# Optimization experiments

Hardware: AMD Instinct MI355X
Metric: run time of the kernel (lower is better)

The kernel has to match this reference:

```python
import jax, jax.numpy as jnp
import numpy as np

N, E, F, DH, R = 50000, 800000, 128, 128, 6  # nodes, edges, in-feat, hidden, relations (heads=1)
EPS = 1e-5
NEG_SLOPE = 0.01


def setup_inputs() -> dict:
    key = jax.random.key(0)
    ks = jax.random.split(key, 20)
    sF = 1.0 / np.sqrt(F)
    sD = 1.0 / np.sqrt(DH)
    return {
        "x": jax.random.normal(ks[0], (N, F), dtype=jnp.float32),
        "edge_index": jax.random.randint(ks[1], (2, E), 0, N, dtype=jnp.int64),
        "edge_type": jax.random.randint(ks[2], (E,), 0, R, dtype=jnp.int64),
        # RGCNConv params
        "rgcn_w": jax.random.normal(ks[3], (R, F, DH), dtype=jnp.float32) * sF,
        "rgcn_root": jax.random.normal(ks[4], (F, DH), dtype=jnp.float32) * sF,
        "rgcn_bias": jnp.zeros((DH,), dtype=jnp.float32),
        # TransformerConv params (heads=1, concat=True)
        "wq": jax.random.normal(ks[5], (DH, DH), dtype=jnp.float32) * sD,
        "bq": jnp.zeros((DH,), dtype=jnp.float32),
        "wk": jax.random.normal(ks[6], (DH, DH), dtype=jnp.float32) * sD,
        "bk": jnp.zeros((DH,), dtype=jnp.float32),
        "wv": jax.random.normal(ks[7], (DH, DH), dtype=jnp.float32) * sD,
        "bv": jnp.zeros((DH,), dtype=jnp.float32),
        "wskip": jax.random.normal(ks[8], (DH, DH), dtype=jnp.float32) * sD,
        "bskip": jnp.zeros((DH,), dtype=jnp.float32),
        # BatchNorm1d params (training-mode batch stats)
        "bn_gamma": jnp.ones((DH,), dtype=jnp.float32),
        "bn_beta": jnp.zeros((DH,), dtype=jnp.float32),
    }


def _rgcn(x, src, dst, edge_type, w, root, bias):
    # PyG RGCNConv: per-relation mean aggregation of x_j @ W_r over incoming edges, + root + bias
    out = x @ root + bias  # [N, DH]
    for r in range(R):
        m = (edge_type == r)
        xw = x @ w[r]  # [N, DH]
        msg = jnp.where(m[:, None], xw[src], 0.0)  # [E, DH]
        s = jax.ops.segment_sum(msg, dst, num_segments=N)
        cnt = jax.ops.segment_sum(m.astype(x.dtype), dst, num_segments=N)
        out = out + s / jnp.maximum(cnt, 1.0)[:, None]
    return out


def _transformer_conv(x, src, dst, wq, bq, wk, bk, wv, bv, wskip, bskip):
    # PyG TransformerConv, heads=1: edge-softmax attention over incoming edges + skip projection
    q = x @ wq + bq  # [N, DH]
    k = x @ wk + bk
    v = x @ wv + bv
    score = jnp.sum(q[dst] * k[src], axis=-1) / jnp.sqrt(jnp.asarray(DH, x.dtype))  # [E]
    smax = jax.ops.segment_max(score, dst, num_segments=N)  # -inf for empty segments (unused)
    a = jnp.exp(score - smax[dst])
    denom = jax.ops.segment_sum(a, dst, num_segments=N)
    alpha = a / denom[dst]  # every edge's dst has >=1 edge, denom > 0
    agg = jax.ops.segment_sum(alpha[:, None] * v[src], dst, num_segments=N)  # [N, DH]
    return agg + (x @ wskip + bskip)


def reference(x, edge_index, edge_type, rgcn_w, rgcn_root, rgcn_bias,
              wq, bq, wk, bk, wv, bv, wskip, bskip, bn_gamma, bn_beta):
    src, dst = edge_index[0], edge_index[1]
    h = _rgcn(x, src, dst, edge_type, rgcn_w, rgcn_root, rgcn_bias)
    h = _transformer_conv(h, src, dst, wq, bq, wk, bk, wv, bv, wskip, bskip)
    # BatchNorm1d (training: batch statistics, biased variance)
    mu = jnp.mean(h, axis=0)
    var = jnp.mean(jnp.square(h - mu), axis=0)
    h = bn_gamma * (h - mu) * jax.lax.rsqrt(var + EPS) + bn_beta
    return jnp.where(h > 0, h, NEG_SLOPE * h)
```

## Files before the change

### kernel.cpp

```cpp
#include <hip/hip_runtime.h>
#include <hip/hip_bf16.h>
#include <math.h>

#define FDIM 128
#define NREL 6

typedef _Float16 half8 __attribute__((ext_vector_type(8)));
typedef _Float16 h16x2 __attribute__((ext_vector_type(2)));
typedef float f32x4 __attribute__((ext_vector_type(4)));

#if __has_builtin(__builtin_amdgcn_fdot2)
#define FDOT2(A, B, C) __builtin_amdgcn_fdot2((A), (B), (C), false)
#else
#define FDOT2(A, B, C) ((float)(A)[0] * (float)(B)[0] + ((float)(A)[1] * (float)(B)[1] + (C)))
#endif

static __device__ __forceinline__ unsigned short f2h(float f) {
  union { _Float16 h; unsigned short u; } p; p.h = (_Float16)f; return p.u;
}

__global__ void cvt_x_kernel(const float* __restrict__ x, unsigned short* __restrict__ xh,
                             int n4) {
  int i = blockIdx.x * 256 + threadIdx.x;
  if (i < n4) {
    float4 v = ((const float4*)x)[i];
    union { _Float16 h[4]; uint2 u; } p;
    p.h[0] = (_Float16)v.x; p.h[1] = (_Float16)v.y;
    p.h[2] = (_Float16)v.z; p.h[3] = (_Float16)v.w;
    ((uint2*)xh)[i] = p.u;
  }
}

__global__ void cvt_wr_kernel(const float* __restrict__ root, const float* __restrict__ w,
                              unsigned short* __restrict__ bt) {
  int i = blockIdx.x * 256 + threadIdx.x;
  if (i < 896 * 128) {
    int n = i / 896, kk = i - n * 896;
    float v = (kk < 128) ? root[kk * 128 + n] : w[(long long)(kk - 128) * 128 + n];
    bt[i] = f2h(v);
  }
}

struct WPtrs { const float* W[4]; };
__global__ void cvt_wq_kernel(WPtrs wp, unsigned short* __restrict__ bt) {
  int i = blockIdx.x * 256 + threadIdx.x;
  if (i < 4 * 128 * 128) {
    int z = i >> 14;
    int r = i & 16383;
    int n = r >> 7, kk = r & 127;
    bt[i] = f2h(wp.W[z][kk * 128 + n]);
  }
}

struct GArgs {
  const unsigned short* Ax;
  const unsigned short* Aagg;
  const unsigned short* Bt;
  const float* bias[4];
  unsigned short* qh; unsigned short* kh; unsigned short* vh; float* sk;
  unsigned short* h;
  int M, K;
};

template <int MODE>
__launch_bounds__(256)
__global__ void gemm_mfma(GArgs g) {
  __shared__ unsigned short Ah[64 * 64];
  __shared__ unsigned short Bh[128 * 64];
  const int tid = threadIdx.x;
  const int lane = tid & 63;
  const int wid = tid >> 6;
  const int wm = wid >> 1, wn = wid & 1;
  const int lr = lane & 15, lk = lane >> 4;
  const int m0 = blockIdx.x * 64;
  const int z = (MODE == 1) ? blockIdx.z : 0;
  const unsigned short* Bt = g.Bt + (long long)z * 128 * g.K;
  const int K = g.K;
  const int M = g.M;

  f32x4 acc[2][4];
#pragma unroll
  for (int a = 0; a < 2; ++a)
#pragma unroll
    for (int b = 0; b < 4; ++b) { acc[a][b][0] = 0.f; acc[a][b][1] = 0.f; acc[a][b][2] = 0.f; acc[a][b][3] = 0.f; }

  for (int k0 = 0; k0 < K; k0 += 64) {
    __syncthreads();
#pragma unroll
    for (int p = 0; p < 2; ++p) {
      int idx = tid + 256 * p;
      int r = idx >> 3, c = idx & 7;
      int row = m0 + r; if (row > M - 1) row = M - 1;
      const unsigned short* srcp;
      if (MODE == 0)
        srcp = (k0 < 128) ? (g.Ax + (long long)row * 128 + k0 + c * 8)
                          : (g.Aagg + (long long)row * 768 + (k0 - 128) + c * 8);
      else
        srcp = g.Ax + (long long)row * 128 + k0 + c * 8;
      uint4 u = *(const uint4*)srcp;
      ((uint4*)Ah)[r * 8 + (c ^ (r & 7))] = u;
    }
#pragma unroll
    for (int p = 0; p < 4; ++p) {
      int idx = tid + 256 * p;
      int rn = idx >> 3, c = idx & 7;
      uint4 u = *(const uint4*)(Bt + (long long)rn * K + k0 + c * 8);
      ((uint4*)Bh)[rn * 8 + (c ^ (rn & 7))] = u;
    }
    __syncthreads();
#pragma unroll
    for (int ks = 0; ks < 2; ++ks) {
      half8 a[2], b[4];
#pragma unroll
      for (int fm = 0; fm < 2; ++fm) {
        int row = wm * 32 + fm * 16 + lr;
        a[fm] = *(const half8*)&((uint4*)Ah)[row * 8 + ((ks * 4 + lk) ^ (row & 7))];
      }
#pragma unroll
      for (int fn = 0; fn < 4; ++fn) {
        int col = wn * 64 + fn * 16 + lr;
        b[fn] = *(const half8*)&((uint4*)Bh)[col * 8 + ((ks * 4 + lk) ^ (col & 7))];
      }
#pragma unroll
      for (int fm = 0; fm < 2; ++fm)
#pragma unroll
        for (int fn = 0; fn < 4; ++fn)
          acc[fm][fn] = __builtin_amdgcn_mfma_f32_16x16x32_f16(a[fm], b[fn], acc[fm][fn], 0, 0, 0);
    }
  }

  const float CF = 0.08838834764831845f * 1.4426950408889634f;
  const float* bias = (MODE == 0) ? g.bias[0] : g.bias[z];
#pragma unroll
  for (int fm = 0; fm < 2; ++fm) {
#pragma unroll
    for (int fn = 0; fn < 4; ++fn) {
      int col = wn * 64 + fn * 16 + lr;
      float bv = bias[col];
#pragma unroll
      for (int j = 0; j < 4; ++j) {
        int row = m0 + wm * 32 + fm * 16 + lk * 4 + j;
        if (row < M) {
          float vv = acc[fm][fn][j] + bv;
          long long off = (long long)row * 128 + col;
          if (MODE == 0) {
            g.h[off] = f2h(vv);
          } else {
            if (z == 0) g.qh[off] = f2h(vv * CF);
            else if (z == 1) g.kh[off] = f2h(vv);
            else if (z == 2) g.vh[off] = f2h(vv);
            else g.sk[off] = vv;
          }
        }
      }
    }
  }
}

__global__ void hist_kernel(const int* __restrict__ dst, const int* __restrict__ etype,
                            int* __restrict__ cnt, int E) {
  int e = blockIdx.x * blockDim.x + threadIdx.x;
  if (e < E) atomicAdd(&cnt[dst[e] * NREL + etype[e]], 1);
}

__launch_bounds__(1024)
__global__ void scan1(const int* __restrict__ deg, int* __restrict__ incl,
                      int* __restrict__ part, int n) {
  __shared__ int sh[1024];
  int tid = threadIdx.x;
  int i = blockIdx.x * 1024 + tid;
  sh[tid] = (i < n) ? deg[i] : 0;
  __syncthreads();
  for (int o = 1; o < 1024; o <<= 1) {
    int t = (tid >= o) ? sh[tid - o] : 0;
    __syncthreads();
    sh[tid] += t;
    __syncthreads();
  }
  if (i < n) incl[i] = sh[tid];
  if (tid == 1023) part[blockIdx.x] = sh[1023];
}

__global__ void scan2(int* part, int nb) {
  int lane = threadIdx.x;
  int run = 0;
  for (int b0 = 0; b0 < nb; b0 += 64) {
    int i = b0 + lane;
    int orig = (i < nb) ? part[i] : 0;
    int v = orig;
#pragma unroll
    for (int o = 1; o < 64; o <<= 1) {
      int t = __shfl_up(v, o);
      if (lane >= o) v += t;
    }
    if (i < nb) part[i] = run + v - orig;
    run += __shfl(v, 63);
  }
}

__global__ void scan3(const int* __restrict__ incl, const int* __restrict__ part,
                      int* __restrict__ offs, int n) {
  int i = blockIdx.x * blockDim.x + threadIdx.x;
  if (i < n) {
    offs[i + 1] = incl[i] + part[i >> 10];
    if (i == 0) offs[0] = 0;
  }
}

__global__ void scatter_kernel(const int* __restrict__ src, const int* __restrict__ dst,
                               const int* __restrict__ etype, const int* __restrict__ offs6,
                               int* __restrict__ cur, int* __restrict__ csrc, int E) {
  int e = blockIdx.x * blockDim.x + threadIdx.x;
  if (e < E) {
    int key = dst[e] * NREL + etype[e];
    int p = offs6[key] + atomicAdd(&cur[key], 1);
    csrc[p] = src[e];
  }
}

__launch_bounds__(256)
__global__ void rgcn_agg(const unsigned short* __restrict__ xh, const int* __restrict__ offs6,
                         const int* __restrict__ csrc,
                         unsigned short* __restrict__ aggh, int N) {
  int node = blockIdx.x * 4 + (threadIdx.x >> 6);
  if (node >= N) return;
  int lane = threadIdx.x & 63;
  const int* bp = offs6 + node * NREL;
  const int b0 = bp[0];
  int bn0 = bp[1], bn1 = bp[2], bn2 = bp[3], bn3 = bp[4], bn4 = bp[5], bn5 = bp[6];
  const int b6 = bn5;
  unsigned* ap = (unsigned*)(aggh + (long long)node * (NREL * FDIM)) + lane;

  float tx = 0.f, ty = 0.f;
  float px = 0.f, py = 0.f;
  int bprev = b0, snaps = 0;

#define FLUSH(EPOS)                                                          \
  while (snaps < NREL && bn0 == (EPOS)) {                                    \
    int cnt_ = (EPOS) - bprev;                                               \
    float inv_ = cnt_ ? 1.f / (float)cnt_ : 0.f;                             \
    union { _Float16 h[2]; unsigned u; } pk_;                                \
    pk_.h[0] = (_Float16)((tx - px) * inv_);                                 \
    pk_.h[1] = (_Float16)((ty - py) * inv_);                                 \
    *ap = pk_.u; ap += 64;                                                   \
    px = tx; py = ty; bprev = (EPOS); ++snaps;                               \
    bn0 = bn1; bn1 = bn2; bn2 = bn3; bn3 = bn4; bn4 = bn5;                   \
  }

#define EAT(XU)                                                              \
  {                                                                          \
    union { unsigned u; _Float16 h[2]; } c_; c_.u = (XU);                    \
    tx += (float)c_.h[0]; ty += (float)c_.h[1];                              \
  }

  FLUSH(b0)
  int e = b0;
  for (; e + 8 <= b6; e += 8) {
    unsigned x0 = ((const unsigned*)(xh + (long long)csrc[e + 0] * FDIM))[lane];
    unsigned x1 = ((const unsigned*)(xh + (long long)csrc[e + 1] * FDIM))[lane];
    unsigned x2 = ((const unsigned*)(xh + (long long)csrc[e + 2] * FDIM))[lane];
    unsigned x3 = ((const unsigned*)(xh + (long long)csrc[e + 3] * FDIM))[lane];
    unsigned x4 = ((const unsigned*)(xh + (long long)csrc[e + 4] * FDIM))[lane];
    unsigned x5 = ((const unsigned*)(xh + (long long)csrc[e + 5] * FDIM))[lane];
    unsigned x6 = ((const unsigned*)(xh + (long long)csrc[e + 6] * FDIM))[lane];
    unsigned x7 = ((const unsigned*)(xh + (long long)csrc[e + 7] * FDIM))[lane];
    EAT(x0) FLUSH(e + 1)
    EAT(x1) FLUSH(e + 2)
    EAT(x2) FLUSH(e + 3)
    EAT(x3) FLUSH(e + 4)
    EAT(x4) FLUSH(e + 5)
    EAT(x5) FLUSH(e + 6)
    EAT(x6) FLUSH(e + 7)
    EAT(x7) FLUSH(e + 8)
  }
  for (; e < b6; ++e) {
    unsigned xv = ((const unsigned*)(xh + (long long)csrc[e] * FDIM))[lane];
    EAT(xv) FLUSH(e + 1)
  }
#undef EAT
#undef FLUSH
}

__launch_bounds__(256)
__global__ void attn_kernel(const unsigned short* __restrict__ qh,
                            const unsigned short* __restrict__ kh,
                            const unsigned short* __restrict__ vh,
                            const int* __restrict__ offs6, const int* __restrict__ csrc,
                            float* __restrict__ out, int N) {
  int node = blockIdx.x * 4 + (threadIdx.x >> 6);
  if (node >= N) return;
  int lane = threadIdx.x & 63;
  int start = offs6[node * NREL], end = offs6[node * NREL + NREL];
  int deg = end - start;
  if (deg <= 0) return;

  const int g16 = lane >> 4;
  const int f = lane & 15;

  union U4 { uint4 u; h16x2 h[4]; };
  U4 qf; qf.u = *(const uint4*)(qh + (long long)node * FDIM + f * 8);

  float m = -INFINITY, den = 0.f, acc0 = 0.f, acc1 = 0.f;

#define LOADQ(E0, S0, S1, S2, S3, KU, V0, V1, V2, V3)                        \
  {                                                                          \
    S0 = csrc[(E0) + (g16 ^ 0)];                                             \
    S1 = csrc[(E0) + (g16 ^ 1)];                                             \
    S2 = csrc[(E0) + (g16 ^ 2)];                                             \
    S3 = csrc[(E0) + (g16 ^ 3)];                                             \
    KU = *(const uint4*)(kh + (long long)S0 * FDIM + f * 8);                 \
    V0 = ((const unsigned*)(vh + (long long)S0 * FDIM))[lane];               \
    V1 = ((const unsigned*)(vh + (long long)S1 * FDIM))[lane];               \
    V2 = ((const unsigned*)(vh + (long long)S2 * FDIM))[lane];               \
    V3 = ((const unsigned*)(vh + (long long)S3 * FDIM))[lane];               \
  }

#define PROCESS(KU, V0, V1, V2, V3, MASKED, M0, M1, M2, M3)                  \
  {                                                                          \
    U4 kf; kf.u = KU;                                                        \
    float pd = FDOT2(qf.h[0], kf.h[0], 0.f);                                 \
    pd = FDOT2(qf.h[1], kf.h[1], pd);                                        \
    pd = FDOT2(qf.h[2], kf.h[2], pd);                                        \
    pd = FDOT2(qf.h[3], kf.h[3], pd);                                        \
    pd += __shfl_xor(pd, 1);  pd += __shfl_xor(pd, 2);                       \
    pd += __shfl_xor(pd, 4);  pd += __shfl_xor(pd, 8);                       \
    float sc0 = pd;                                        \
    float sc1 = __shfl_xor(pd, 16);                        \
    float sc2 = __shfl_xor(pd, 32);                        \
    float sc3 = __shfl_xor(pd, 48);                        \
    if (MASKED) {                                                            \
      if (!(M0)) sc0 = -INFINITY;                                            \
      if (!(M1)) sc1 = -INFINITY;                                            \
      if (!(M2)) sc2 = -INFINITY;                                            \
      if (!(M3)) sc3 = -INFINITY;                                            \
    }                                                                        \
    float mx = fmaxf(fmaxf(sc0, sc1), fmaxf(sc2, sc3));                      \
    float mn = fmaxf(m, mx);                                                 \
    float scl = exp2f(m - mn);                                               \
    float a0 = exp2f(sc0 - mn), a1 = exp2f(sc1 - mn);                        \
    float a2 = exp2f(sc2 - mn), a3 = exp2f(sc3 - mn);                        \
    den = den * scl + ((a0 + a1) + (a2 + a3));                               \
    union { unsigned u; _Float16 h[2]; } w0, w1, w2, w3;                     \
    w0.u = V0; w1.u = V1; w2.u = V2; w3.u = V3;                              \
    acc0 = acc0 * scl + a0 * (float)w0.h[0] + a1 * (float)w1.h[0]            \
                      + a2 * (float)w2.h[0] + a3 * (float)w3.h[0];           \
    acc1 = acc1 * scl + a0 * (float)w0.h[1] + a1 * (float)w1.h[1]            \
                      + a2 * (float)w2.h[1] + a3 * (float)w3.h[1];           \
    m = mn;                                                                  \
  }

  int nfull4 = deg & ~3;
  int e = start;
  if (nfull4 > 0) {
    int sA0, sA1, sA2, sA3; uint4 kA; unsigned vA0, vA1, vA2, vA3;
    LOADQ(e, sA0, sA1, sA2, sA3, kA, vA0, vA1, vA2, vA3)
    for (; e < start + nfull4; e += 4) {
      int sB0, sB1, sB2, sB3; uint4 kB; unsigned vB0, vB1, vB2, vB3;
      bool more = (e + 4 < start + nfull4);
      if (more) LOADQ(e + 4, sB0, sB1, sB2, sB3, kB, vB0, vB1, vB2, vB3)
      PROCESS(kA, vA0, vA1, vA2, vA3, false, 1, 1, 1, 1)
      if (more) { kA = kB; vA0 = vB0; vA1 = vB1; vA2 = vB2; vA3 = vB3; }
    }
  }
  int rem = deg & 3;
  if (rem) {
    int e0 = start + nfull4;
    int j0 = g16 ^ 0, j1 = g16 ^ 1, j2 = g16 ^ 2, j3 = g16 ^ 3;
    int sT0 = csrc[e0 + (j0 < rem ? j0 : 0)];
    int sT1 = csrc[e0 + (j1 < rem ? j1 : 0)];
    int sT2 = csrc[e0 + (j2 < rem ? j2 : 0)];
    int sT3 = csrc[e0 + (j3 < rem ? j3 : 0)];
    uint4 kT = *(const uint4*)(kh + (long long)sT0 * FDIM + f * 8);
    unsigned vT0 = ((const unsigned*)(vh + (long long)sT0 * FDIM))[lane];
    unsigned vT1 = ((const unsigned*)(vh + (long long)sT1 * FDIM))[lane];
    unsigned vT2 = ((const unsigned*)(vh + (long long)sT2 * FDIM))[lane];
    unsigned vT3 = ((const unsigned*)(vh + (long long)sT3 * FDIM))[lane];
    PROCESS(kT, vT0, vT1, vT2, vT3, true, j0 < rem, j1 < rem, j2 < rem, j3 < rem)
  }
#undef LOADQ
#undef PROCESS

  float inv = 1.f / den;
  float2* op = (float2*)(out + (long long)node * FDIM);
  float2 o = op[lane];
  o.x += acc0 * inv;
  o.y += acc1 * inv;
  op[lane] = o;
}

__launch_bounds__(128)
__global__ void bn_stats(const float* __restrict__ x, float* __restrict__ gsum,
                         float* __restrict__ gsq, int N) {
  int d = threadIdx.x;
  float s = 0.f, qq = 0.f;
  for (int r = blockIdx.x; r < N; r += gridDim.x) {
    float vv = x[(long long)r * FDIM + d];
    s += vv;
    qq += vv * vv;
  }
  atomicAdd(&gsum[d], s);
  atomicAdd(&gsq[d], qq);
}

__global__ void bn_final(const float* __restrict__ gsum, const float* __restrict__ gsq,
                         const float* __restrict__ gamma, const float* __restrict__ beta,
                         float* __restrict__ ss, int N) {
  int d = threadIdx.x;
  if (d < FDIM) {
    float mean = gsum[d] / (float)N;
    float var = gsq[d] / (float)N - mean * mean;
    var = fmaxf(var, 0.f);
    float sc = gamma[d] * rsqrtf(var + 1e-5f);
    ss[d] = sc;
    ss[FDIM + d] = beta[d] - mean * sc;
  }
}

__global__ void bn_apply(float* __restrict__ x, const float* __restrict__ ss, long long total4) {
  long long i = (long long)blockIdx.x * blockDim.x + threadIdx.x;
  if (i < total4) {
    int d0 = (int)((i * 4) & (FDIM - 1));
    float4 vv = ((const float4*)x)[i];
    float y0 = ss[d0 + 0] * vv.x + ss[FDIM + d0 + 0];
    float y1 = ss[d0 + 1] * vv.y + ss[FDIM + d0 + 1];
    float y2 = ss[d0 + 2] * vv.z + ss[FDIM + d0 + 2];
    float y3 = ss[d0 + 3] * vv.w + ss[FDIM + d0 + 3];
    vv.x = (y0 > 0.f) ? y0 : 0.01f * y0;
    vv.y = (y1 > 0.f) ? y1 : 0.01f * y1;
    vv.z = (y2 > 0.f) ? y2 : 0.01f * y2;
    vv.w = (y3 > 0.f) ? y3 : 0.01f * y3;
    ((float4*)x)[i] = vv;
  }
}

extern "C" void kernel_launch(void* const* d_in, const int* in_sizes, int n_in,
                              void* d_out, int out_size, void* d_ws, size_t ws_size,
                              hipStream_t stream) {
  const float* x         = (const float*)d_in[0];
  const int*   ei        = (const int*)d_in[1];
  const int*   etype     = (const int*)d_in[2];
  const float* rgcn_w    = (const float*)d_in[3];
  const float* rgcn_root = (const float*)d_in[4];
  const float* rgcn_bias = (const float*)d_in[5];
  const float* wq = (const float*)d_in[6];  const float* bq = (const float*)d_in[7];
  const float* wk = (const float*)d_in[8];  const float* bk = (const float*)d_in[9];
  const float* wv = (const float*)d_in[10]; const float* bv = (const float*)d_in[11];
  const float* wsk = (const float*)d_in[12]; const float* bsk = (const float*)d_in[13];
  const float* gamma = (const float*)d_in[14]; const float* beta = (const float*)d_in[15];

  const int N = in_sizes[0] / FDIM;
  const int E = in_sizes[1] / 2;
  const int* src = ei;
  const int* dst = ei + E;
  const int NK = N * NREL;

  char* base = (char*)d_ws;
  size_t off = 0;
  auto alloc = [&](size_t bytes) -> char* {
    char* p = base + off;
    off += (bytes + 255) & ~(size_t)255;
    return p;
  };
  unsigned short* aggh = (unsigned short*)alloc((size_t)N * (NREL * FDIM) * 2);
  unsigned short* qbuf = aggh;
  unsigned short* kbuf = aggh + (size_t)N * FDIM;
  unsigned short* vbuf = aggh + 2 * (size_t)N * FDIM;
  unsigned short* xh   = (unsigned short*)alloc((size_t)N * FDIM * 2);
  unsigned short* hh   = (unsigned short*)alloc((size_t)N * FDIM * 2);
  unsigned short* btR  = (unsigned short*)alloc((size_t)896 * 128 * 2);
  unsigned short* btQ  = (unsigned short*)alloc((size_t)4 * 128 * 128 * 2);
  int* cnt6 = (int*)alloc((size_t)2 * NK * 4);
  int* cur  = cnt6 + NK;
  int* offs6 = (int*)alloc((size_t)(NK + 1) * 4);
  int* incl = (int*)alloc((size_t)NK * 4);
  int* part = (int*)alloc((size_t)512 * 4);
  int* csrc = (int*)alloc((size_t)E * 4);
  float* gsum = (float*)alloc((size_t)(128 + 128 + 256) * 4);
  float* gsq  = gsum + FDIM;
  float* ss   = gsum + 2 * FDIM;

  float* out = (float*)d_out;

  hipMemsetAsync(cnt6, 0, (size_t)2 * NK * sizeof(int), stream);
  hipMemsetAsync(gsum, 0, (size_t)2 * FDIM * sizeof(float), stream);

  int n4 = N * FDIM / 4;
  cvt_x_kernel<<<(n4 + 255) / 256, 256, 0, stream>>>(x, xh, n4);
  cvt_wr_kernel<<<(896 * 128 + 255) / 256, 256, 0, stream>>>(rgcn_root, rgcn_w, btR);
  WPtrs wp; wp.W[0] = wq; wp.W[1] = wk; wp.W[2] = wv; wp.W[3] = wsk;
  cvt_wq_kernel<<<(4 * 128 * 128 + 255) / 256, 256, 0, stream>>>(wp, btQ);

  hist_kernel<<<(E + 255) / 256, 256, 0, stream>>>(dst, etype, cnt6, E);
  int nb = (NK + 1023) / 1024;
  scan1<<<nb, 1024, 0, stream>>>(cnt6, incl, part, NK);
  scan2<<<1, 64, 0, stream>>>(part, nb);
  scan3<<<(NK + 255) / 256, 256, 0, stream>>>(incl, part, offs6, NK);
  scatter_kernel<<<(E + 255) / 256, 256, 0, stream>>>(src, dst, etype, offs6, cur, csrc, E);

  const int nodeBlocks = (N + 3) / 4;
  const int gemmBlocks = (N + 63) / 64;

  rgcn_agg<<<nodeBlocks, 256, 0, stream>>>(xh, offs6, csrc, aggh, N);

  GArgs g0 = {};
  g0.Ax = xh; g0.Aagg = aggh; g0.Bt = btR;
  g0.bias[0] = rgcn_bias;
  g0.h = hh; g0.M = N; g0.K = 896;
  gemm_mfma<0><<<dim3(gemmBlocks, 1, 1), 256, 0, stream>>>(g0);

  GArgs g1 = {};
  g1.Ax = hh; g1.Bt = btQ;
  g1.bias[0] = bq; g1.bias[1] = bk; g1.bias[2] = bv; g1.bias[3] = bsk;
  g1.qh = qbuf; g1.kh = kbuf; g1.vh = vbuf; g1.sk = out;
  g1.M = N; g1.K = 128;
  gemm_mfma<1><<<dim3(gemmBlocks, 1, 4), 256, 0, stream>>>(g1);

  attn_kernel<<<nodeBlocks, 256, 0, stream>>>(qbuf, kbuf, vbuf, offs6, csrc, out, N);

  bn_stats<<<512, 128, 0, stream>>>(out, gsum, gsq, N);
  bn_final<<<1, 128, 0, stream>>>(gsum, gsq, gamma, beta, ss, N);
  long long total4 = (long long)N * FDIM / 4;
  bn_apply<<<(int)((total4 + 255) / 256), 256, 0, stream>>>(out, ss, total4);
}
```

Before: 334.2 us.

## Enlarge GEMM M-tile to 128, use direct global-to-LDS loads, prescale CSR indices

The MFMA GEMM now computes 128-row tiles per block, with each warp holding a 4x4 accumulator grid. It stages A and B tiles straight into LDS using global_load_lds with the XOR swizzle applied to the source address, which removes the register round trip. Separately, the CSR source indices are stored pre-shifted by 8 (the byte offset of a 128-half row), so the gather kernels skip the 64-bit multiply in address math. The larger tile means more registers per thread and half as many blocks, which may lower occupancy. The shifted indices overflow int if N*256 exceeds 2^31, which is fine at this N.

Result: slower. 349.7 us (+4.7%).

```diff
diff --git a/kernel.cpp b/kernel.cpp
--- a/kernel.cpp
+++ b/kernel.cpp
@@ -14,6 +14,11 @@
 #else
 #define FDOT2(A, B, C) ((float)(A)[0] * (float)(B)[0] + ((float)(A)[1] * (float)(B)[1] + (C)))
 #endif
+
+#define GLOAD_LDS16(GP, LP)                                                    \
+  __builtin_amdgcn_global_load_lds(                                            \
+      (const __attribute__((address_space(1))) unsigned int*)(const void*)(GP),\
+      (__attribute__((address_space(3))) unsigned int*)(void*)(LP), 16, 0, 0)
 
 static __device__ __forceinline__ unsigned short f2h(float f) {
   union { _Float16 h; unsigned short u; } p; p.h = (_Float16)f; return p.u;
@@ -65,55 +70,57 @@
 template <int MODE>
 __launch_bounds__(256)
 __global__ void gemm_mfma(GArgs g) {
-  __shared__ unsigned short Ah[64 * 64];
+  __shared__ unsigned short Ah[128 * 64];
   __shared__ unsigned short Bh[128 * 64];
   const int tid = threadIdx.x;
   const int lane = tid & 63;
   const int wid = tid >> 6;
   const int wm = wid >> 1, wn = wid & 1;
   const int lr = lane & 15, lk = lane >> 4;
-  const int m0 = blockIdx.x * 64;
+  const int m0 = blockIdx.x * 128;
   const int z = (MODE == 1) ? blockIdx.z : 0;
   const unsigned short* Bt = g.Bt + (long long)z * 128 * g.K;
   const int K = g.K;
   const int M = g.M;
 
-  f32x4 acc[2][4];
-#pragma unroll
-  for (int a = 0; a < 2; ++a)
-#pragma unroll
-    for (int b = 0; b < 4; ++b) { acc[a][b][0] = 0.f; acc[a][b][1] = 0.f; acc[a][b][2] = 0.f; acc[a][b][3] = 0.f; }
+  f32x4 acc[4][4];
+#pragma unroll
+  for (int a = 0; a < 4; ++a)
+#pragma unroll
+    for (int b = 0; b < 4; ++b) {
+      acc[a][b][0] = 0.f; acc[a][b][1] = 0.f; acc[a][b][2] = 0.f; acc[a][b][3] = 0.f;
+    }
 
   for (int k0 = 0; k0 < K; k0 += 64) {
     __syncthreads();
 #pragma unroll
-    for (int p = 0; p < 2; ++p) {
-      int idx = tid + 256 * p;
-      int r = idx >> 3, c = idx & 7;
+    for (int p = 0; p < 4; ++p) {
+      int u = (p * 4 + wid) * 64 + lane;
+      int r = u >> 3, c = u & 7;
       int row = m0 + r; if (row > M - 1) row = M - 1;
       const unsigned short* srcp;
       if (MODE == 0)
-        srcp = (k0 < 128) ? (g.Ax + (long long)row * 128 + k0 + c * 8)
-                          : (g.Aagg + (long long)row * 768 + (k0 - 128) + c * 8);
+        srcp = (k0 < 128) ? (g.Ax + (long long)row * 128 + k0)
+                          : (g.Aagg + (long long)row * 768 + (k0 - 128));
       else
-        srcp = g.Ax + (long long)row * 128 + k0 + c * 8;
-      uint4 u = *(const uint4*)srcp;
-      ((uint4*)Ah)[r * 8 + (c ^ (r & 7))] = u;
+        srcp = g.Ax + (long long)row * 128 + k0;
+      srcp += (c ^ (r & 7)) * 8;
+      GLOAD_LDS16(srcp, &Ah[(p * 4 + wid) * 512]);
     }
 #pragma unroll
     for (int p = 0; p < 4; ++p) {
-      int idx = tid + 256 * p;
-      int rn = idx >> 3, c = idx & 7;
-      uint4 u = *(const uint4*)(Bt + (long long)rn * K + k0 + c * 8);
-      ((uint4*)Bh)[rn * 8 + (c ^ (rn & 7))] = u;
+      int u = (p * 4 + wid) * 64 + lane;
+      int rn = u >> 3, c = u & 7;
+      const unsigned short* srcp = Bt + (long long)rn * K + k0 + (c ^ (rn & 7)) * 8;
+      GLOAD_LDS16(srcp, &Bh[(p * 4 + wid) * 512]);
     }
     __syncthreads();
 #pragma unroll
     for (int ks = 0; ks < 2; ++ks) {
-      half8 a[2], b[4];
-#pragma unroll
-      for (int fm = 0; fm < 2; ++fm) {
-        int row = wm * 32 + fm * 16 + lr;
+      half8 a[4], b[4];
+#pragma unroll
+      for (int fm = 0; fm < 4; ++fm) {
+        int row = wm * 64 + fm * 16 + lr;
         a[fm] = *(const half8*)&((uint4*)Ah)[row * 8 + ((ks * 4 + lk) ^ (row & 7))];
       }
 #pragma unroll
@@ -122,7 +129,7 @@
         b[fn] = *(const half8*)&((uint4*)Bh)[col * 8 + ((ks * 4 + lk) ^ (col & 7))];
       }
 #pragma unroll
-      for (int fm = 0; fm < 2; ++fm)
+      for (int fm = 0; fm < 4; ++fm)
 #pragma unroll
         for (int fn = 0; fn < 4; ++fn)
           acc[fm][fn] = __builtin_amdgcn_mfma_f32_16x16x32_f16(a[fm], b[fn], acc[fm][fn], 0, 0, 0);
@@ -132,14 +139,14 @@
   const float CF = 0.08838834764831845f * 1.4426950408889634f;
   const float* bias = (MODE == 0) ? g.bias[0] : g.bias[z];
 #pragma unroll
-  for (int fm = 0; fm < 2; ++fm) {
+  for (int fm = 0; fm < 4; ++fm) {
 #pragma unroll
     for (int fn = 0; fn < 4; ++fn) {
       int col = wn * 64 + fn * 16 + lr;
       float bv = bias[col];
 #pragma unroll
       for (int j = 0; j < 4; ++j) {
-        int row = m0 + wm * 32 + fm * 16 + lk * 4 + j;
+        int row = m0 + wm * 64 + fm * 16 + lk * 4 + j;
         if (row < M) {
           float vv = acc[fm][fn][j] + bv;
           long long off = (long long)row * 128 + col;
@@ -214,7 +221,7 @@
   if (e < E) {
     int key = dst[e] * NREL + etype[e];
     int p = offs6[key] + atomicAdd(&cur[key], 1);
-    csrc[p] = src[e];
+    csrc[p] = src[e] << 8;
   }
 }
 
@@ -225,6 +232,7 @@
   int node = blockIdx.x * 4 + (threadIdx.x >> 6);
   if (node >= N) return;
   int lane = threadIdx.x & 63;
+  const char* xc = (const char*)xh;
   const int* bp = offs6 + node * NREL;
   const int b0 = bp[0];
   int bn0 = bp[1], bn1 = bp[2], bn2 = bp[3], bn3 = bp[4], bn4 = bp[5], bn5 = bp[6];
@@ -256,14 +264,14 @@
   FLUSH(b0)
   int e = b0;
   for (; e + 8 <= b6; e += 8) {
-    unsigned x0 = ((const unsigned*)(xh + (long long)csrc[e + 0] * FDIM))[lane];
-    unsigned x1 = ((const unsigned*)(xh + (long long)csrc[e + 1] * FDIM))[lane];
-    unsigned x2 = ((const unsigned*)(xh + (long long)csrc[e + 2] * FDIM))[lane];
-    unsigned x3 = ((const unsigned*)(xh + (long long)csrc[e + 3] * FDIM))[lane];
-    unsigned x4 = ((const unsigned*)(xh + (long long)csrc[e + 4] * FDIM))[lane];
-    unsigned x5 = ((const unsigned*)(xh + (long long)csrc[e + 5] * FDIM))[lane];
-    unsigned x6 = ((const unsigned*)(xh + (long long)csrc[e + 6] * FDIM))[lane];
-    unsigned x7 = ((const unsigned*)(xh + (long long)csrc[e + 7] * FDIM))[lane];
+    unsigned x0 = ((const unsigned*)(xc + csrc[e + 0]))[lane];
+    unsigned x1 = ((const unsigned*)(xc + csrc[e + 1]))[lane];
+    unsigned x2 = ((const unsigned*)(xc + csrc[e + 2]))[lane];
+    unsigned x3 = ((const unsigned*)(xc + csrc[e + 3]))[lane];
+    unsigned x4 = ((const unsigned*)(xc + csrc[e + 4]))[lane];
+    unsigned x5 = ((const unsigned*)(xc + csrc[e + 5]))[lane];
+    unsigned x6 = ((const unsigned*)(xc + csrc[e + 6]))[lane];
+    unsigned x7 = ((const unsigned*)(xc + csrc[e + 7]))[lane];
     EAT(x0) FLUSH(e + 1)
     EAT(x1) FLUSH(e + 2)
     EAT(x2) FLUSH(e + 3)
@@ -274,7 +282,7 @@
     EAT(x7) FLUSH(e + 8)
   }
   for (; e < b6; ++e) {
-    unsigned xv = ((const unsigned*)(xh + (long long)csrc[e] * FDIM))[lane];
+    unsigned xv = ((const unsigned*)(xc + csrc[e]))[lane];
     EAT(xv) FLUSH(e + 1)
   }
 #undef EAT
@@ -296,6 +304,8 @@
 
   const int g16 = lane >> 4;
   const int f = lane & 15;
+  const char* kc = (const char*)kh;
+  const char* vc = (const char*)vh;
 
   union U4 { uint4 u; h16x2 h[4]; };
   U4 qf; qf.u = *(const uint4*)(qh + (long long)node * FDIM + f * 8);
@@ -308,11 +318,11 @@
     S1 = csrc[(E0) + (g16 ^ 1)];                                             \
     S2 = csrc[(E0) + (g16 ^ 2)];                                             \
     S3 = csrc[(E0) + (g16 ^ 3)];                                             \
-    KU = *(const uint4*)(kh + (long long)S0 * FDIM + f * 8);                 \
-    V0 = ((const unsigned*)(vh + (long long)S0 * FDIM))[lane];               \
-    V1 = ((const unsigned*)(vh + (long long)S1 * FDIM))[lane];               \
-    V2 = ((const unsigned*)(vh + (long long)S2 * FDIM))[lane];               \
-    V3 = ((const unsigned*)(vh + (long long)S3 * FDIM))[lane];               \
+    KU = *(const uint4*)(kc + S0 + f * 16);                                  \
+    V0 = ((const unsigned*)(vc + S0))[lane];                                 \
+    V1 = ((const unsigned*)(vc + S1))[lane];                                 \
+    V2 = ((const unsigned*)(vc + S2))[lane];                                 \
+    V3 = ((const unsigned*)(vc + S3))[lane];                                 \
   }
 
 #define PROCESS(KU, V0, V1, V2, V3, MASKED, M0, M1, M2, M3)                  \
@@ -370,11 +380,11 @@
     int sT1 = csrc[e0 + (j1 < rem ? j1 : 0)];
     int sT2 = csrc[e0 + (j2 < rem ? j2 : 0)];
     int sT3 = csrc[e0 + (j3 < rem ? j3 : 0)];
-    uint4 kT = *(const uint4*)(kh + (long long)sT0 * FDIM + f * 8);
-    unsigned vT0 = ((const unsigned*)(vh + (long long)sT0 * FDIM))[lane];
-    unsigned vT1 = ((const unsigned*)(vh + (long long)sT1 * FDIM))[lane];
-    unsigned vT2 = ((const unsigned*)(vh + (long long)sT2 * FDIM))[lane];
-    unsigned vT3 = ((const unsigned*)(vh + (long long)sT3 * FDIM))[lane];
+    uint4 kT = *(const uint4*)(kc + sT0 + f * 16);
+    unsigned vT0 = ((const unsigned*)(vc + sT0))[lane];
+    unsigned vT1 = ((const unsigned*)(vc + sT1))[lane];
+    unsigned vT2 = ((const unsigned*)(vc + sT2))[lane];
+    unsigned vT3 = ((const unsigned*)(vc + sT3))[lane];
     PROCESS(kT, vT0, vT1, vT2, vT3, true, j0 < rem, j1 < rem, j2 < rem, j3 < rem)
   }
 #undef LOADQ
@@ -498,7 +508,7 @@
   scatter_kernel<<<(E + 255) / 256, 256, 0, stream>>>(src, dst, etype, offs6, cur, csrc, E);
 
   const int nodeBlocks = (N + 3) / 4;
-  const int gemmBlocks = (N + 63) / 64;
+  const int gemmBlocks = (N + 127) / 128;
 
   rgcn_agg<<<nodeBlocks, 256, 0, stream>>>(xh, offs6, csrc, aggh, N);
 
```
